# Kernel tuning notes

Hardware: AMD Instinct MI355X
Metric: run time of the kernel (lower is better)

The kernel has to match this reference:

```python
import math
import jax, jax.numpy as jnp
import numpy as np

HEAD_SIZE = 64
MAX_LEN = 1024
ENT_HEADS = 2
REL_HEADS = 24
NEG_BIG = 1e12


def rope_tables(max_pos=MAX_LEN, head_size=HEAD_SIZE):
    # coord_dim=2 -> table built with d_hid = head_size // 2
    d = head_size // 2
    pos = jnp.arange(max_pos, dtype=jnp.float32)[:, None]            # [P,1]
    div = jnp.exp(jnp.arange(0, d, 2, dtype=jnp.float32) * (-math.log(10000.0) / d))  # [d/2]
    ang = pos * div                                                   # [P, d/2]
    # table[:,1::2]=cos, table[:,::2]=sin; repeat_interleave(2) == jnp.repeat(...,2)
    cosp = jnp.repeat(jnp.cos(ang), 2, axis=-1)                       # [P, d]
    sinp = jnp.repeat(jnp.sin(ang), 2, axis=-1)                       # [P, d]
    return cosp, sinp


def apply_rope2d(qw, cosp, sinp, xp, yp):
    # qw: [b,s,h,hs]; xp,yp: [b,s] int positions
    cos = jnp.concatenate([cosp[xp], cosp[yp]], axis=-1)[:, :, None, :]  # [b,s,1,hs]
    sin = jnp.concatenate([sinp[xp], sinp[yp]], axis=-1)[:, :, None, :]
    qw2 = jnp.stack([-qw[..., 1::2], qw[..., ::2]], axis=-1).reshape(qw.shape)
    return qw * cos + qw2 * sin


def gp_layer(x, W, b, heads, mask, xp, yp, cosp, sinp, tril):
    hs = HEAD_SIZE
    bsz, s, _ = x.shape
    # dense then torch.chunk(heads)+stack == reshape to [b,s,heads,2*hs]
    seq = (x @ W + b).reshape(bsz, s, heads, 2 * hs)
    qw, kw = seq[..., :hs], seq[..., hs:]
    qw = apply_rope2d(qw, cosp, sinp, xp, yp)
    kw = apply_rope2d(kw, cosp, sinp, xp, yp)
    logits = jnp.einsum('bmhd,bnhd->bhmn', qw, kw)                    # [b,h,s,s]
    pad = (mask[:, None, :, None] > 0) & (mask[:, None, None, :] > 0)
    logits = jnp.where(pad, logits, -jnp.inf)
    if tril:
        logits = logits - jnp.tril(jnp.ones((s, s), logits.dtype), -1) * NEG_BIG
    return logits / (hs ** 0.5)


def setup_inputs() -> dict:
    key = jax.random.key(0)
    ks = jax.random.split(key, 8)
    b, s, h = 4, 512, 1024
    return {
        'last_hidden_state': jax.random.normal(ks[0], (b, s, h), dtype=jnp.float32),
        'attention_mask': jnp.ones((b, s), dtype=jnp.int32),
        'x_pos': jax.random.randint(ks[1], (b, s), 0, MAX_LEN, dtype=jnp.int32),
        'y_pos': jax.random.randint(ks[2], (b, s), 0, MAX_LEN, dtype=jnp.int32),
        'W_ent': jax.random.normal(ks[3], (h, ENT_HEADS * 2 * HEAD_SIZE), dtype=jnp.float32) * 0.02,
        'b_ent': jnp.zeros((ENT_HEADS * 2 * HEAD_SIZE,), dtype=jnp.float32),
        'W_head': jax.random.normal(ks[4], (h, REL_HEADS * 2 * HEAD_SIZE), dtype=jnp.float32) * 0.02,
        'b_head': jnp.zeros((REL_HEADS * 2 * HEAD_SIZE,), dtype=jnp.float32),
        'W_tail': jax.random.normal(ks[5], (h, REL_HEADS * 2 * HEAD_SIZE), dtype=jnp.float32) * 0.02,
        'b_tail': jnp.zeros((REL_HEADS * 2 * HEAD_SIZE,), dtype=jnp.float32),
    }


def reference(last_hidden_state, attention_mask, x_pos, y_pos,
              W_ent, b_ent, W_head, b_head, W_tail, b_tail):
    cosp, sinp = rope_tables()
    ent = gp_layer(last_hidden_state, W_ent, b_ent, ENT_HEADS,
                   attention_mask, x_pos, y_pos, cosp, sinp, tril=True)
    head = gp_layer(last_hidden_state, W_head, b_head, REL_HEADS,
                    attention_mask, x_pos, y_pos, cosp, sinp, tril=False)
    tail = gp_layer(last_hidden_state, W_tail, b_tail, REL_HEADS,
                    attention_mask, x_pos, y_pos, cosp, sinp, tril=False)
    return jnp.concatenate([ent, head, tail], axis=1)  # [b, 2+24+24, s, s]
```

## Files before the change

### kernel.cpp

```cpp
#include <hip/hip_runtime.h>
#include <hip/hip_bf16.h>
#include <math.h>

#define NUM_B 4
#define SEQ 512
#define HID 1024
#define NH 50
#define NCOL 6400
#define M_TOK 2048

typedef short bf16x8_t __attribute__((ext_vector_type(8)));
typedef float f32x4_t __attribute__((ext_vector_type(4)));

__device__ __forceinline__ unsigned short f2bf(float f) {
    union { float f; unsigned int u; } v; v.f = f;
    unsigned int u = v.u;
    u += 0x7fffu + ((u >> 16) & 1u);
    return (unsigned short)(u >> 16);
}
__device__ __forceinline__ float bf2f(unsigned short h) {
    union { unsigned int u; float f; } v; v.u = ((unsigned int)h) << 16;
    return v.f;
}

__device__ __forceinline__ void gload_lds16(const void* g, void* l) {
    __builtin_amdgcn_global_load_lds(
        (__attribute__((address_space(1))) unsigned int*)(unsigned long long)g,
        (__attribute__((address_space(3))) unsigned int*)(unsigned long long)(uintptr_t)l,
        16, 0, 0);
}

__global__ void k_tables(float* cosT, float* sinT) {
    int idx = blockIdx.x * blockDim.x + threadIdx.x;
    int p = idx >> 5, j = idx & 31;
    float div = expf(-logf(10000.f) * (float)(2 * (j >> 1)) / 32.f);
    float ang = (float)p * div;
    cosT[idx] = cosf(ang);
    sinT[idx] = sinf(ang);
}

__global__ void k_cvt_x(const float* __restrict__ x, unsigned short* __restrict__ xb) {
    int i = blockIdx.x * blockDim.x + threadIdx.x;
    float4 v = ((const float4*)x)[i];
    ushort4 o;
    o.x = f2bf(v.x); o.y = f2bf(v.y); o.z = f2bf(v.z); o.w = f2bf(v.w);
    ((ushort4*)xb)[i] = o;
}

__global__ void k_cvt_w(const float* __restrict__ W, unsigned short* __restrict__ Wt,
                        int N, int n_off) {
    __shared__ float t[32][33];
    int n = blockIdx.x * 32 + threadIdx.x;
    int k = blockIdx.y * 32 + threadIdx.y;
    t[threadIdx.y][threadIdx.x] = W[(size_t)k * N + n];
    __syncthreads();
    int on = blockIdx.x * 32 + threadIdx.y;
    int ok = blockIdx.y * 32 + threadIdx.x;
    Wt[(size_t)(n_off + on) * HID + ok] = f2bf(t[threadIdx.x][threadIdx.y]);
}

__global__ void k_bias(const float* __restrict__ be, const float* __restrict__ bh,
                       const float* __restrict__ bt, float* __restrict__ ball) {
    int i = blockIdx.x * blockDim.x + threadIdx.x;
    if (i < 256) ball[i] = be[i];
    else if (i < 3328) ball[i] = bh[i - 256];
    else ball[i] = bt[i - 3328];
}

__global__ __launch_bounds__(256) void k_gemm1(const unsigned short* __restrict__ A,
                                               const unsigned short* __restrict__ Bt,
                                               const float* __restrict__ bias,
                                               unsigned short* __restrict__ seq) {
    __shared__ __align__(16) unsigned short As[128 * 64];
    __shared__ __align__(16) unsigned short Bs[128 * 64];
    int tid = threadIdx.x;
    int wave = tid >> 6, lane = tid & 63;
    int l15 = lane & 15, q = lane >> 4;
    int m0 = blockIdx.x * 128, n0 = blockIdx.y * 128;
    int wm = (wave >> 1) * 64, wn = (wave & 1) * 64;

    f32x4_t acc[4][4];
#pragma unroll
    for (int i = 0; i < 4; i++)
#pragma unroll
        for (int j = 0; j < 4; j++) acc[i][j] = (f32x4_t){0.f, 0.f, 0.f, 0.f};

    for (int k0 = 0; k0 < HID; k0 += 64) {
        __syncthreads();
#pragma unroll
        for (int it = 0; it < 4; ++it) {
            int c = it * 256 + tid;
            int r = c >> 3, cl = c & 7;
            int cg = cl ^ (r & 7);
            gload_lds16(A + (size_t)(m0 + r) * HID + k0 + cg * 8, As + c * 8);
            gload_lds16(Bt + (size_t)(n0 + r) * HID + k0 + cg * 8, Bs + c * 8);
        }
        __syncthreads();
#pragma unroll
        for (int ks = 0; ks < 2; ++ks) {
            bf16x8_t af[4], bfr[4];
#pragma unroll
            for (int i = 0; i < 4; i++) {
                int r = wm + i * 16 + l15;
                int cl = (ks * 4 + q) ^ (r & 7);
                af[i] = *(const bf16x8_t*)&As[r * 64 + cl * 8];
            }
#pragma unroll
            for (int j = 0; j < 4; j++) {
                int r = wn + j * 16 + l15;
                int cl = (ks * 4 + q) ^ (r & 7);
                bfr[j] = *(const bf16x8_t*)&Bs[r * 64 + cl * 8];
            }
#pragma unroll
            for (int i = 0; i < 4; i++)
#pragma unroll
                for (int j = 0; j < 4; j++)
                    acc[i][j] = __builtin_amdgcn_mfma_f32_16x16x32_bf16(af[i], bfr[j], acc[i][j], 0, 0, 0);
        }
    }
#pragma unroll
    for (int j = 0; j < 4; j++) {
        int n = n0 + wn + j * 16 + l15;
        float bv = bias[n];
#pragma unroll
        for (int i = 0; i < 4; i++)
#pragma unroll
            for (int r = 0; r < 4; r++) {
                int m = m0 + wm + i * 16 + q * 4 + r;
                seq[(size_t)m * NCOL + n] = f2bf(acc[i][j][r] + bv);
            }
    }
}

__global__ void k_rope(unsigned short* __restrict__ seq, const int* __restrict__ xp,
                       const int* __restrict__ yp, const float* __restrict__ cosT,
                       const float* __restrict__ sinT) {
    int t = blockIdx.x * blockDim.x + threadIdx.x;
    int m = t / 3200;
    int p = t - m * 3200;
    int n = p * 2;
    int dd = n & 63;
    int pos = (dd < 32) ? xp[m] : yp[m];
    int tj = dd & 31;
    float c = cosT[pos * 32 + tj];
    float s = sinT[pos * 32 + tj];
    unsigned int v = *(unsigned int*)&seq[(size_t)m * NCOL + n];
    float q0 = bf2f((unsigned short)(v & 0xffffu));
    float q1 = bf2f((unsigned short)(v >> 16));
    float r0 = q0 * c - q1 * s;
    float r1 = q1 * c + q0 * s;
    unsigned int o = (unsigned int)f2bf(r0) | ((unsigned int)f2bf(r1) << 16);
    *(unsigned int*)&seq[(size_t)m * NCOL + n] = o;
}

__global__ __launch_bounds__(256) void k_attn(const unsigned short* __restrict__ seq,
                                              const int* __restrict__ mask,
                                              float* __restrict__ out) {
    __shared__ __align__(16) unsigned short Qs[128 * 64];
    __shared__ __align__(16) unsigned short Ks[128 * 64];
    int tid = threadIdx.x;
    int bh = blockIdx.z;
    int b = bh / NH, h = bh - b * NH;
    int m0 = blockIdx.x * 128, n0 = blockIdx.y * 128;
    const unsigned short* qbase = seq + (size_t)b * SEQ * NCOL + h * 128;

#pragma unroll
    for (int it = 0; it < 4; ++it) {
        int c = it * 256 + tid;
        int r = c >> 3, cl = c & 7;
        int cg = cl ^ (r & 7);
        gload_lds16(qbase + (size_t)(m0 + r) * NCOL + cg * 8, Qs + c * 8);
        gload_lds16(qbase + (size_t)(n0 + r) * NCOL + 64 + cg * 8, Ks + c * 8);
    }
    __syncthreads();

    int wave = tid >> 6, lane = tid & 63;
    int l15 = lane & 15, q = lane >> 4;
    int wm = (wave >> 1) * 64, wn = (wave & 1) * 64;

    f32x4_t acc[4][4];
#pragma unroll
    for (int i = 0; i < 4; i++)
#pragma unroll
        for (int j = 0; j < 4; j++) acc[i][j] = (f32x4_t){0.f, 0.f, 0.f, 0.f};

#pragma unroll
    for (int ks = 0; ks < 2; ++ks) {
        bf16x8_t af[4], bfr[4];
#pragma unroll
        for (int i = 0; i < 4; i++) {
            int r = wm + i * 16 + l15;
            int cl = (ks * 4 + q) ^ (r & 7);
            af[i] = *(const bf16x8_t*)&Qs[r * 64 + cl * 8];
        }
#pragma unroll
        for (int j = 0; j < 4; j++) {
            int r = wn + j * 16 + l15;
            int cl = (ks * 4 + q) ^ (r & 7);
            bfr[j] = *(const bf16x8_t*)&Ks[r * 64 + cl * 8];
        }
#pragma unroll
        for (int i = 0; i < 4; i++)
#pragma unroll
            for (int j = 0; j < 4; j++)
                acc[i][j] = __builtin_amdgcn_mfma_f32_16x16x32_bf16(af[i], bfr[j], acc[i][j], 0, 0, 0);
    }

    const int* mrow = mask + b * SEQ;
    bool ent = (h < 2);
    size_t obase = (size_t)bh * SEQ * SEQ;
#pragma unroll
    for (int j = 0; j < 4; j++) {
        int n = n0 + wn + j * 16 + l15;
        int maskn = mrow[n];
#pragma unroll
        for (int i = 0; i < 4; i++)
#pragma unroll
            for (int r = 0; r < 4; r++) {
                int m = m0 + wm + i * 16 + q * 4 + r;
                float v = acc[i][j][r] * 0.125f;
                if (ent && m > n) v -= 1.25e11f;
                if (mrow[m] == 0 || maskn == 0) v = -INFINITY;
                out[obase + (size_t)m * SEQ + n] = v;
            }
    }
}

extern "C" void kernel_launch(void* const* d_in, const int* in_sizes, int n_in,
                              void* d_out, int out_size, void* d_ws, size_t ws_size,
                              hipStream_t stream) {
    const float* x      = (const float*)d_in[0];
    const int*   mask   = (const int*)d_in[1];
    const int*   xp     = (const int*)d_in[2];
    const int*   yp     = (const int*)d_in[3];
    const float* W_ent  = (const float*)d_in[4];
    const float* b_ent  = (const float*)d_in[5];
    const float* W_head = (const float*)d_in[6];
    const float* b_head = (const float*)d_in[7];
    const float* W_tail = (const float*)d_in[8];
    const float* b_tail = (const float*)d_in[9];
    float* out = (float*)d_out;

    char* ws = (char*)d_ws;
    size_t off = 0;
    auto alloc = [&](size_t bytes) {
        void* p = ws + off;
        off += (bytes + 255) & ~(size_t)255;
        return p;
    };
    float* cosT = (float*)alloc(32768 * 4);
    float* sinT = (float*)alloc(32768 * 4);
    unsigned short* xb  = (unsigned short*)alloc((size_t)M_TOK * HID * 2);
    unsigned short* Wt  = (unsigned short*)alloc((size_t)NCOL * HID * 2);
    float* ball = (float*)alloc(NCOL * 4);
    unsigned short* seq = (unsigned short*)alloc((size_t)M_TOK * NCOL * 2);

    k_tables<<<128, 256, 0, stream>>>(cosT, sinT);
    k_cvt_x<<<2048, 256, 0, stream>>>(x, xb);
    dim3 tb(32, 32);
    k_cvt_w<<<dim3(8, 32), tb, 0, stream>>>(W_ent, Wt, 256, 0);
    k_cvt_w<<<dim3(96, 32), tb, 0, stream>>>(W_head, Wt, 3072, 256);
    k_cvt_w<<<dim3(96, 32), tb, 0, stream>>>(W_tail, Wt, 3072, 3328);
    k_bias<<<25, 256, 0, stream>>>(b_ent, b_head, b_tail, ball);
    k_gemm1<<<dim3(16, 50), 256, 0, stream>>>(xb, Wt, ball, seq);
    k_rope<<<25600, 256, 0, stream>>>(seq, xp, yp, cosT, sinT);
    k_attn<<<dim3(4, 4, 200), 256, 0, stream>>>(seq, mask, out);
}
```

Before: 371.3 us.

## Fuse RoPE into GEMM epilogue, swap MFMA operands for vectorized stores, merge prep kernels

Applies RoPE inside the projection GEMM epilogue, which removes the separate rope kernel and its full read-modify-write pass over the seq buffer. Swapping the MFMA operand order puts four consecutive columns in each lane, so both the GEMM and attention epilogues can issue vector stores (ushort4 and float4) instead of scalar ones. The small setup kernels (table, x conversion, bias) are merged into one launch, and the three weight transposes into another, which cuts launch count. The cos/sin table is packed as float2. The attention output write of about 200 MB dominates, and float4 stores should make it more coalesced.

```diff
diff --git a/kernel.cpp b/kernel.cpp
--- a/kernel.cpp
+++ b/kernel.cpp
@@ -18,10 +18,6 @@
     u += 0x7fffu + ((u >> 16) & 1u);
     return (unsigned short)(u >> 16);
 }
-__device__ __forceinline__ float bf2f(unsigned short h) {
-    union { unsigned int u; float f; } v; v.u = ((unsigned int)h) << 16;
-    return v.f;
-}
 
 __device__ __forceinline__ void gload_lds16(const void* g, void* l) {
     __builtin_amdgcn_global_load_lds(
@@ -30,46 +26,56 @@
         16, 0, 0);
 }
 
-__global__ void k_tables(float* cosT, float* sinT) {
-    int idx = blockIdx.x * blockDim.x + threadIdx.x;
-    int p = idx >> 5, j = idx & 31;
-    float div = expf(-logf(10000.f) * (float)(2 * (j >> 1)) / 32.f);
-    float ang = (float)p * div;
-    cosT[idx] = cosf(ang);
-    sinT[idx] = sinf(ang);
-}
-
-__global__ void k_cvt_x(const float* __restrict__ x, unsigned short* __restrict__ xb) {
-    int i = blockIdx.x * blockDim.x + threadIdx.x;
-    float4 v = ((const float4*)x)[i];
-    ushort4 o;
-    o.x = f2bf(v.x); o.y = f2bf(v.y); o.z = f2bf(v.z); o.w = f2bf(v.w);
-    ((ushort4*)xb)[i] = o;
-}
-
-__global__ void k_cvt_w(const float* __restrict__ W, unsigned short* __restrict__ Wt,
-                        int N, int n_off) {
+__global__ void k_prep(const float* __restrict__ x, unsigned short* __restrict__ xb,
+                       float2* __restrict__ csT,
+                       const float* __restrict__ be, const float* __restrict__ bh,
+                       const float* __restrict__ bt, float* __restrict__ ball) {
+    int bid = blockIdx.x, tid = threadIdx.x;
+    if (bid < 2048) {
+        int i = bid * 256 + tid;
+        float4 v = ((const float4*)x)[i];
+        ushort4 o;
+        o.x = f2bf(v.x); o.y = f2bf(v.y); o.z = f2bf(v.z); o.w = f2bf(v.w);
+        ((ushort4*)xb)[i] = o;
+    } else if (bid < 2112) {
+        int idx = (bid - 2048) * 256 + tid;
+        int p = idx >> 4, t2 = idx & 15;
+        float ang = (float)p * expf(-logf(10000.f) * (float)(2 * t2) / 32.f);
+        csT[idx] = make_float2(cosf(ang), sinf(ang));
+    } else {
+        int i = (bid - 2112) * 256 + tid;
+        if (i < 6400) {
+            float v;
+            if (i < 256) v = be[i];
+            else if (i < 3328) v = bh[i - 256];
+            else v = bt[i - 3328];
+            ball[i] = v;
+        }
+    }
+}
+
+__global__ void k_cvt_w(const float* __restrict__ We, const float* __restrict__ Wh,
+                        const float* __restrict__ Wl, unsigned short* __restrict__ Wo) {
     __shared__ float t[32][33];
     int n = blockIdx.x * 32 + threadIdx.x;
+    const float* W; int Nw, nc;
+    if (n < 256)       { W = We; Nw = 256;  nc = n; }
+    else if (n < 3328) { W = Wh; Nw = 3072; nc = n - 256; }
+    else               { W = Wl; Nw = 3072; nc = n - 3328; }
     int k = blockIdx.y * 32 + threadIdx.y;
-    t[threadIdx.y][threadIdx.x] = W[(size_t)k * N + n];
+    t[threadIdx.y][threadIdx.x] = W[(size_t)k * Nw + nc];
     __syncthreads();
     int on = blockIdx.x * 32 + threadIdx.y;
     int ok = blockIdx.y * 32 + threadIdx.x;
-    Wt[(size_t)(n_off + on) * HID + ok] = f2bf(t[threadIdx.x][threadIdx.y]);
-}
-
-__global__ void k_bias(const float* __restrict__ be, const float* __restrict__ bh,
-                       const float* __restrict__ bt, float* __restrict__ ball) {
-    int i = blockIdx.x * blockDim.x + threadIdx.x;
-    if (i < 256) ball[i] = be[i];
-    else if (i < 3328) ball[i] = bh[i - 256];
-    else ball[i] = bt[i - 3328];
+    Wo[(size_t)on * HID + ok] = f2bf(t[threadIdx.x][threadIdx.y]);
 }
 
 __global__ __launch_bounds__(256) void k_gemm1(const unsigned short* __restrict__ A,
                                                const unsigned short* __restrict__ Bt,
                                                const float* __restrict__ bias,
+                                               const int* __restrict__ xp,
+                                               const int* __restrict__ yp,
+                                               const float2* __restrict__ csT,
                                                unsigned short* __restrict__ seq) {
     __shared__ __align__(16) unsigned short As[128 * 64];
     __shared__ __align__(16) unsigned short Bs[128 * 64];
@@ -115,42 +121,37 @@
             for (int i = 0; i < 4; i++)
 #pragma unroll
                 for (int j = 0; j < 4; j++)
-                    acc[i][j] = __builtin_amdgcn_mfma_f32_16x16x32_bf16(af[i], bfr[j], acc[i][j], 0, 0, 0);
-        }
-    }
-#pragma unroll
-    for (int j = 0; j < 4; j++) {
-        int n = n0 + wn + j * 16 + l15;
-        float bv = bias[n];
-#pragma unroll
-        for (int i = 0; i < 4; i++)
-#pragma unroll
-            for (int r = 0; r < 4; r++) {
-                int m = m0 + wm + i * 16 + q * 4 + r;
-                seq[(size_t)m * NCOL + n] = f2bf(acc[i][j][r] + bv);
-            }
-    }
-}
-
-__global__ void k_rope(unsigned short* __restrict__ seq, const int* __restrict__ xp,
-                       const int* __restrict__ yp, const float* __restrict__ cosT,
-                       const float* __restrict__ sinT) {
-    int t = blockIdx.x * blockDim.x + threadIdx.x;
-    int m = t / 3200;
-    int p = t - m * 3200;
-    int n = p * 2;
-    int dd = n & 63;
-    int pos = (dd < 32) ? xp[m] : yp[m];
-    int tj = dd & 31;
-    float c = cosT[pos * 32 + tj];
-    float s = sinT[pos * 32 + tj];
-    unsigned int v = *(unsigned int*)&seq[(size_t)m * NCOL + n];
-    float q0 = bf2f((unsigned short)(v & 0xffffu));
-    float q1 = bf2f((unsigned short)(v >> 16));
-    float r0 = q0 * c - q1 * s;
-    float r1 = q1 * c + q0 * s;
-    unsigned int o = (unsigned int)f2bf(r0) | ((unsigned int)f2bf(r1) << 16);
-    *(unsigned int*)&seq[(size_t)m * NCOL + n] = o;
+                    acc[i][j] = __builtin_amdgcn_mfma_f32_16x16x32_bf16(bfr[j], af[i], acc[i][j], 0, 0, 0);
+        }
+    }
+
+    float4 bj[4];
+#pragma unroll
+    for (int j = 0; j < 4; j++)
+        bj[j] = *(const float4*)&bias[n0 + wn + j * 16 + q * 4];
+#pragma unroll
+    for (int i = 0; i < 4; i++) {
+        int m = m0 + wm + i * 16 + l15;
+        int posx = xp[m] * 16, posy = yp[m] * 16;
+#pragma unroll
+        for (int j = 0; j < 4; j++) {
+            float v0 = acc[i][j][0] + bj[j].x;
+            float v1 = acc[i][j][1] + bj[j].y;
+            float v2 = acc[i][j][2] + bj[j].z;
+            float v3 = acc[i][j][3] + bj[j].w;
+            int pos = (j < 2) ? posx : posy;
+            int t2 = (j & 1) * 8 + q * 2;
+            float2 cs0 = csT[pos + t2];
+            float2 cs1 = csT[pos + t2 + 1];
+            float r0 = v0 * cs0.x - v1 * cs0.y;
+            float r1 = v1 * cs0.x + v0 * cs0.y;
+            float r2 = v2 * cs1.x - v3 * cs1.y;
+            float r3 = v3 * cs1.x + v2 * cs1.y;
+            ushort4 o;
+            o.x = f2bf(r0); o.y = f2bf(r1); o.z = f2bf(r2); o.w = f2bf(r3);
+            *(ushort4*)&seq[(size_t)m * NCOL + n0 + wn + j * 16 + q * 4] = o;
+        }
+    }
 }
 
 __global__ __launch_bounds__(256) void k_attn(const unsigned short* __restrict__ seq,
@@ -203,26 +204,40 @@
         for (int i = 0; i < 4; i++)
 #pragma unroll
             for (int j = 0; j < 4; j++)
-                acc[i][j] = __builtin_amdgcn_mfma_f32_16x16x32_bf16(af[i], bfr[j], acc[i][j], 0, 0, 0);
+                acc[i][j] = __builtin_amdgcn_mfma_f32_16x16x32_bf16(bfr[j], af[i], acc[i][j], 0, 0, 0);
     }
 
     const int* mrow = mask + b * SEQ;
     bool ent = (h < 2);
     size_t obase = (size_t)bh * SEQ * SEQ;
-#pragma unroll
-    for (int j = 0; j < 4; j++) {
-        int n = n0 + wn + j * 16 + l15;
-        int maskn = mrow[n];
-#pragma unroll
-        for (int i = 0; i < 4; i++)
-#pragma unroll
-            for (int r = 0; r < 4; r++) {
-                int m = m0 + wm + i * 16 + q * 4 + r;
-                float v = acc[i][j][r] * 0.125f;
-                if (ent && m > n) v -= 1.25e11f;
-                if (mrow[m] == 0 || maskn == 0) v = -INFINITY;
-                out[obase + (size_t)m * SEQ + n] = v;
+    int4 mn[4];
+#pragma unroll
+    for (int j = 0; j < 4; j++)
+        mn[j] = *(const int4*)&mrow[n0 + wn + j * 16 + q * 4];
+#pragma unroll
+    for (int i = 0; i < 4; i++) {
+        int m = m0 + wm + i * 16 + l15;
+        bool mz = (mrow[m] == 0);
+#pragma unroll
+        for (int j = 0; j < 4; j++) {
+            int nb = n0 + wn + j * 16 + q * 4;
+            float4 v;
+            v.x = acc[i][j][0] * 0.125f;
+            v.y = acc[i][j][1] * 0.125f;
+            v.z = acc[i][j][2] * 0.125f;
+            v.w = acc[i][j][3] * 0.125f;
+            if (ent) {
+                if (m > nb)     v.x -= 1.25e11f;
+                if (m > nb + 1) v.y -= 1.25e11f;
+                if (m > nb + 2) v.z -= 1.25e11f;
+                if (m > nb + 3) v.w -= 1.25e11f;
             }
+            if (mz || mn[j].x == 0) v.x = -INFINITY;
+            if (mz || mn[j].y == 0) v.y = -INFINITY;
+            if (mz || mn[j].z == 0) v.z = -INFINITY;
+            if (mz || mn[j].w == 0) v.w = -INFINITY;
+            *(float4*)&out[obase + (size_t)m * SEQ + nb] = v;
+        }
     }
 }
 
@@ -248,21 +263,14 @@
         off += (bytes + 255) & ~(size_t)255;
         return p;
     };
-    float* cosT = (float*)alloc(32768 * 4);
-    float* sinT = (float*)alloc(32768 * 4);
+    float2* csT = (float2*)alloc(16384 * 8);
     unsigned short* xb  = (unsigned short*)alloc((size_t)M_TOK * HID * 2);
     unsigned short* Wt  = (unsigned short*)alloc((size_t)NCOL * HID * 2);
     float* ball = (float*)alloc(NCOL * 4);
     unsigned short* seq = (unsigned short*)alloc((size_t)M_TOK * NCOL * 2);
 
-    k_tables<<<128, 256, 0, stream>>>(cosT, sinT);
-    k_cvt_x<<<2048, 256, 0, stream>>>(x, xb);
-    dim3 tb(32, 32);
-    k_cvt_w<<<dim3(8, 32), tb, 0, stream>>>(W_ent, Wt, 256, 0);
-    k_cvt_w<<<dim3(96, 32), tb, 0, stream>>>(W_head, Wt, 3072, 256);
-    k_cvt_w<<<dim3(96, 32), tb, 0, stream>>>(W_tail, Wt, 3072, 3328);
-    k_bias<<<25, 256, 0, stream>>>(b_ent, b_head, b_tail, ball);
-    k_gemm1<<<dim3(16, 50), 256, 0, stream>>>(xb, Wt, ball, seq);
-    k_rope<<<25600, 256, 0, stream>>>(seq, xp, yp, cosT, sinT);
+    k_prep<<<2137, 256, 0, stream>>>(x, xb, csT, b_ent, b_head, b_tail, ball);
+    k_cvt_w<<<dim3(200, 32), dim3(32, 32), 0, stream>>>(W_ent, W_head, W_tail, Wt);
+    k_gemm1<<<dim3(16, 50), 256, 0, stream>>>(xb, Wt, ball, xp, yp, csT, seq);
     k_attn<<<dim3(4, 4, 200), 256, 0, stream>>>(seq, mask, out);
 }
```

Result: faster. 326.5 us (-12.1%).
